# Kernel optimization log

Hardware: AMD Instinct MI355X
Metric: run time of the kernel (lower is better)

Reference implementation:

```python
import jax, jax.numpy as jnp
import numpy as np

KH, KW = 3, 3
KK = KH * KW
PAD = 1
STRIDE = 1


def setup_inputs() -> dict:
    key = jax.random.key(0)
    k1, k2, k3 = jax.random.split(key, 3)
    x = jax.random.normal(k1, (4, 64, 224, 224), jnp.float32)
    weight = jax.random.normal(k2, (64, 64, KH, KW), jnp.float32) * 0.05
    bias = jax.random.normal(k3, (64,), jnp.float32)
    return {"x": x, "weight": weight, "bias": bias}


def reference(x, weight, bias):
    B, C, H, W = x.shape
    # --- conv output (the wrapper delegates this to the wrapped conv) ---
    y = jax.lax.conv_general_dilated(
        x, weight,
        window_strides=(STRIDE, STRIDE),
        padding=((PAD, PAD), (PAD, PAD)),
        dimension_numbers=("NCHW", "OIHW", "NCHW"),
    ) + bias[None, :, None, None]

    # --- zero-count histogram (groups=1; torch code's [:, :, :, 0, 0] indexing
    # selects group 0 / out-channel 0, so only weight[0] matters) ---
    # patches: (B, C*KK, Ho, Wo), channel-major ordering (channel, then kh, kw)
    patches = jax.lax.conv_general_dilated_patches(
        x, (KH, KW), (STRIDE, STRIDE), ((PAD, PAD), (PAD, PAD)))
    Ho, Wo = patches.shape[2], patches.shape[3]
    patches = patches.reshape(B, C, KK, Ho, Wo)
    prod = patches * weight[0].reshape(1, C, KK, 1, 1)  # patch * weight, oc=0
    # num_of_zeros = kk - count_nonzero over the kernel window
    zeros = KK - jnp.count_nonzero(prod, axis=2)  # (B, C, Ho, Wo), int
    # accumulate one_hot(zeros).sum over (batch, h, w) per input channel
    zf = zeros.transpose(1, 0, 2, 3).reshape(C, -1)  # (C, B*Ho*Wo)
    hist = jnp.zeros((C, KK + 1), jnp.float32).at[
        jnp.arange(C)[:, None], zf].add(1.0)
    return y, hist
```

## Files before the change

kernel.cpp:

```cpp
#include <hip/hip_runtime.h>

#define HW 224
#define HW2 50176
#define NCH 64
#define NPIX (4 * HW2)
#define CONV_OUT_ELEMS (4 * NCH * HW2)
#define ZCAP 8192

#define TH 7
#define TW 32
#define LHH 9
#define LWW 34
#define NPOS 306
#define NGRAN (NPOS * 8)

typedef short bf16x8 __attribute__((ext_vector_type(8)));
typedef float f32x4 __attribute__((ext_vector_type(4)));

__device__ __forceinline__ unsigned short f2bf(float f) {
    unsigned u = __float_as_uint(f);
    u += 0x7FFFu + ((u >> 16) & 1u);
    return (unsigned short)(u >> 16);
}

__device__ __forceinline__ void gload16(const unsigned short* src,
                                        unsigned short* dst_uniform) {
    __builtin_amdgcn_global_load_lds(
        (const __attribute__((address_space(1))) unsigned int*)src,
        (__attribute__((address_space(3))) unsigned int*)dst_uniform,
        16, 0, 0);
}


__global__ __launch_bounds__(256) void prep_fused(
    const float* __restrict__ xf, const float* __restrict__ w,
    unsigned short* __restrict__ xbf, unsigned short* __restrict__ wbufA,
    int* __restrict__ zcnt, unsigned int* __restrict__ zlist)
{
    const int tid = threadIdx.x;
    const int bid = blockIdx.x;

    if (bid >= 6272) {
        const int o = (bid - 6272) * 256 + tid;
        if (o < 18 * 2048) {
            const int j    = o & 7;
            const int lane = (o >> 3) & 63;
            const int n    = lane & 15;
            const int q    = lane >> 4;
            const int mg   = (o >> 9) & 3;
            const int k    = o >> 11;
            const int tap  = k >> 1;
            const int half = k & 1;
            const int ci   = half * 32 + q * 8 + j;
            const int co   = mg * 16 + n;
            wbufA[o] = f2bf(w[(co * 64 + ci) * 9 + tap]);
        }
        return;
    }

    const int pix = bid * 32 + (tid >> 3);
    const int oct = tid & 7;
    const int b   = pix / HW2;
    const int rem = pix - b * HW2;
    const float* src = xf + (size_t)(b * NCH + oct * 8) * HW2 + rem;

    float fv[8];
#pragma unroll
    for (int j = 0; j < 8; ++j) fv[j] = src[(size_t)j * HW2];

    bf16x8 v;
#pragma unroll
    for (int j = 0; j < 8; ++j) v[j] = (short)f2bf(fv[j]);
    *reinterpret_cast<bf16x8*>(xbf + (size_t)pix * 64 + oct * 8) = v;

    bool anyz = false;
#pragma unroll
    for (int j = 0; j < 8; ++j) anyz |= (fv[j] == 0.0f);
    if (__builtin_expect(anyz, 0)) {
        const int yy = rem / HW;
        const int xx = rem - yy * HW;
#pragma unroll
        for (int j = 0; j < 8; ++j) {
            if (fv[j] == 0.0f) {
                const int idx = atomicAdd(zcnt, 1);
                if (idx < ZCAP) {
                    const int ci = oct * 8 + j;
                    zlist[idx] = ((unsigned)b << 22) | ((unsigned)ci << 16)
                               | ((unsigned)yy << 8) | (unsigned)xx;
                }
            }
        }
    }
}

__global__ __launch_bounds__(256, 4) void conv_fused(
    const unsigned short* __restrict__ xbf,
    const unsigned short* __restrict__ wbufA,
    const float* __restrict__ bias, float* __restrict__ y)
{
    __shared__ alignas(16) unsigned short xs[NPOS * 64];

    const int tid  = threadIdx.x;
    const int wv   = tid >> 6;
    const int lane = tid & 63;
    const int n    = lane & 15;
    const int q    = lane >> 4;
    const int c0   = blockIdx.x * TW;
    const int r0   = blockIdx.y * TH;
    const int b    = blockIdx.z;

#pragma unroll
    for (int it = 0; it < 10; ++it) {
        const int s = it * 256 + tid;
        if (it < 9 || s < NGRAN) {
            const int pos = s >> 3;
            const int bq  = s & 7;
            const int rr  = pos / LWW;
            const int cc  = pos - rr * LWW;
            const int gy  = r0 + rr - 1;
            const int gx  = c0 + cc - 1;
            const int blk = bq ^ (pos & 7);
            unsigned short* dstb = xs + (size_t)(it * 256 + wv * 64) * 8;
            if ((unsigned)gy < (unsigned)HW && (unsigned)gx < (unsigned)HW) {
                const unsigned short* src =
                    xbf + ((size_t)(b * HW + gy) * HW + gx) * 64 + blk * 8;
                gload16(src, dstb);
            } else {
                *reinterpret_cast<bf16x8*>(xs + (size_t)s * 8) =
                    (bf16x8){0, 0, 0, 0, 0, 0, 0, 0};
            }
        }
    }
    __syncthreads();

    f32x4 acc[4][4];
#pragma unroll
    for (int mg = 0; mg < 4; ++mg)
#pragma unroll
        for (int g = 0; g < 4; ++g) acc[mg][g] = (f32x4){0.f, 0.f, 0.f, 0.f};

    const int rw0 = 2 * wv;
    const int rw1 = (2 * wv + 1 > TH - 1) ? TH - 1 : 2 * wv + 1;

#pragma unroll
    for (int tap = 0; tap < 9; ++tap) {
        const int dh = tap / 3, dw = tap % 3;
#pragma unroll
        for (int half = 0; half < 2; ++half) {
            const int k = tap * 2 + half;
            bf16x8 a[4];
#pragma unroll
            for (int mg = 0; mg < 4; ++mg)
                a[mg] = *reinterpret_cast<const bf16x8*>(
                    wbufA + (k * 4 + mg) * 512 + lane * 8);
#pragma unroll
            for (int g = 0; g < 4; ++g) {
                const int rI  = (g >> 1) ? rw1 : rw0;
                const int pos = (rI + dh) * LWW + (g & 1) * 16 + dw + n;
                const int phys = pos * 8 + ((half * 4 + q) ^ (pos & 7));
                const bf16x8 bf =
                    *reinterpret_cast<const bf16x8*>(xs + phys * 8);
#pragma unroll
                for (int mg = 0; mg < 4; ++mg)
                    acc[mg][g] = __builtin_amdgcn_mfma_f32_16x16x32_bf16(
                        a[mg], bf, acc[mg][g], 0, 0, 0);
            }
        }
    }

#pragma unroll
    for (int g = 0; g < 4; ++g) {
        const int rt = 2 * wv + (g >> 1);
        if (rt < TH) {
            const int row = r0 + rt;
            const int col = c0 + (g & 1) * 16 + n;
#pragma unroll
            for (int mg = 0; mg < 4; ++mg) {
#pragma unroll
                for (int rg = 0; rg < 4; ++rg) {
                    const int co = mg * 16 + q * 4 + rg;
                    y[((size_t)(b * NCH + co) * HW + row) * HW + col] =
                        acc[mg][g][rg] + bias[co];
                }
            }
        }
    }
}

__global__ __launch_bounds__(256) void hist_final(
    const float* __restrict__ x, const float* __restrict__ w,
    const int* __restrict__ zcnt, const unsigned int* __restrict__ zlist,
    float* __restrict__ hist)
{
    __shared__ int lh[640];
    const int tid = threadIdx.x;
    for (int i = tid; i < 640; i += 256) lh[i] = 0;
    __syncthreads();

    if (tid < 64) {
        const int c = tid;
        float wk[9];
#pragma unroll
        for (int k = 0; k < 9; ++k) wk[k] = w[c * 9 + k];
        int bins[10];
#pragma unroll
        for (int k = 0; k < 10; ++k) bins[k] = 0;
#pragma unroll
        for (int rcat = 0; rcat < 3; ++rcat) {
#pragma unroll
            for (int scat = 0; scat < 3; ++scat) {
                int z = 0;
#pragma unroll
                for (int k = 0; k < 9; ++k) {
                    const int kh = k / 3, kw = k % 3;
                    const bool oob =
                        (rcat == 0 && kh == 0) || (rcat == 2 && kh == 2) ||
                        (scat == 0 && kw == 0) || (scat == 2 && kw == 2);
                    z += (oob || wk[k] == 0.0f) ? 1 : 0;
                }
                const int cnt =
                    4 * (rcat == 1 ? 222 : 1) * (scat == 1 ? 222 : 1);
                bins[z] += cnt;
            }
        }
#pragma unroll
        for (int k = 0; k < 10; ++k) lh[c * 10 + k] = bins[k];
    }
    __syncthreads();

    const int L = min(*zcnt, ZCAP);
    for (int p = tid; p < L * 9; p += 256) {
        const int e = p / 9, t = p - e * 9;
        const unsigned ent = zlist[e];
        const int b  = (int)(ent >> 22);
        const int c  = (int)(ent >> 16) & 63;
        const int zy = (int)(ent >> 8) & 255;
        const int zx = (int)ent & 255;
        const int kh = t / 3, kw = t % 3;
        const int r = zy - kh + 1, s = zx - kw + 1;
        if ((unsigned)r >= (unsigned)HW || (unsigned)s >= (unsigned)HW)
            continue;
        bool first = true;
        for (int e2 = 0; e2 < e && first; ++e2) {
            const unsigned ent2 = zlist[e2];
            if ((ent2 >> 16) == (ent >> 16)) {
                const int y2 = (int)(ent2 >> 8) & 255;
                const int x2 = (int)ent2 & 255;
                if ((unsigned)(y2 - r + 1) < 3u && (unsigned)(x2 - s + 1) < 3u)
                    first = false;
            }
        }
        if (!first) continue;

        const float* plane = x + (size_t)(b * NCH + c) * HW2;
        int zb = 0, zt = 0;
#pragma unroll
        for (int k = 0; k < 9; ++k) {
            const int kh2 = k / 3, kw2 = k % 3;
            const int yy = r + kh2 - 1, xx = s + kw2 - 1;
            const bool oob = (unsigned)yy >= (unsigned)HW ||
                             (unsigned)xx >= (unsigned)HW;
            const bool w0 = (w[c * 9 + k] == 0.0f);
            const bool x0 = !oob && (plane[yy * HW + xx] == 0.0f);
            zb += (oob || w0) ? 1 : 0;
            zt += (oob || w0 || x0) ? 1 : 0;
        }
        if (zb != zt) {
            atomicAdd(&lh[c * 10 + zb], -1);
            atomicAdd(&lh[c * 10 + zt], 1);
        }
    }
    __syncthreads();
    for (int i = tid; i < 640; i += 256) hist[i] = (float)lh[i];
}

__global__ void prep_weights_fb(const float* __restrict__ w,
                                unsigned short* __restrict__ wbuf) {
    const int o = blockIdx.x * 256 + threadIdx.x;
    if (o >= 2 * 9 * 4 * 16 * 32) return;
    const int ci = o & 31;
    const int t1 = o >> 5;
    const int co = t1 & 15;
    const int t2 = t1 >> 4;
    const int mg = t2 & 3;
    const int t3 = t2 >> 2;
    const int tap = t3 % 9;
    const int chunk = t3 / 9;
    wbuf[o] = f2bf(w[((mg * 16 + co) * 64 + (chunk * 32 + ci)) * 9 + tap]);
}

__global__ __launch_bounds__(256, 2) void conv_mfma_fb(
    const float* __restrict__ x, const unsigned short* __restrict__ wbuf,
    const float* __restrict__ bias, float* __restrict__ y)
{
    __shared__ alignas(16) unsigned short xs[340 * 32];
    const int tid  = threadIdx.x;
    const int wv   = tid >> 6;
    const int lane = tid & 63;
    const int n    = lane & 15;
    const int q    = lane >> 4;
    const int c0   = blockIdx.x * 32;
    const int r0   = blockIdx.y * 8;
    const int b    = blockIdx.z;

    f32x4 acc[4][4];
#pragma unroll
    for (int mg = 0; mg < 4; ++mg)
#pragma unroll
        for (int g = 0; g < 4; ++g) acc[mg][g] = (f32x4){0.f, 0.f, 0.f, 0.f};

    for (int chunk = 0; chunk < 2; ++chunk) {
        if (chunk) __syncthreads();
        const int ci0 = chunk * 32;
        for (int i = tid; i < 1360; i += 256) {
            const int ci8 = i / 340;
            const int pos = i - ci8 * 340;
            const int r   = pos / 34;
            const int c   = pos - r * 34;
            const int gy  = r0 + r - 1;
            const int gx  = c0 + c - 1;
            bf16x8 v;
            if ((unsigned)gy < (unsigned)HW && (unsigned)gx < (unsigned)HW) {
                const float* src =
                    x + ((size_t)(b * NCH + ci0 + ci8 * 8) * HW + gy) * HW + gx;
#pragma unroll
                for (int j = 0; j < 8; ++j) v[j] = (short)f2bf(src[(size_t)j * HW2]);
            } else {
#pragma unroll
                for (int j = 0; j < 8; ++j) v[j] = 0;
            }
            *reinterpret_cast<bf16x8*>(&xs[pos * 32 + ci8 * 8]) = v;
        }
        __syncthreads();

#pragma unroll
        for (int tap = 0; tap < 9; ++tap) {
            const int dh = tap / 3, dw = tap % 3;
            bf16x8 a[4];
#pragma unroll
            for (int mg = 0; mg < 4; ++mg) {
                const unsigned short* ap =
                    wbuf + ((chunk * 9 + tap) * 4 + mg) * 512 + n * 32 + q * 8;
                a[mg] = *reinterpret_cast<const bf16x8*>(ap);
            }
#pragma unroll
            for (int g = 0; g < 4; ++g) {
                const int rl = 2 * wv + (g >> 1) + dh;
                const int cl = (g & 1) * 16 + dw + n;
                const bf16x8 bf =
                    *reinterpret_cast<const bf16x8*>(&xs[(rl * 34 + cl) * 32 + q * 8]);
#pragma unroll
                for (int mg = 0; mg < 4; ++mg)
                    acc[mg][g] = __builtin_amdgcn_mfma_f32_16x16x32_bf16(
                        a[mg], bf, acc[mg][g], 0, 0, 0);
            }
        }
    }

#pragma unroll
    for (int g = 0; g < 4; ++g) {
        const int row = r0 + 2 * wv + (g >> 1);
        const int col = c0 + (g & 1) * 16 + n;
#pragma unroll
        for (int mg = 0; mg < 4; ++mg) {
#pragma unroll
            for (int rg = 0; rg < 4; ++rg) {
                const int co = mg * 16 + q * 4 + rg;
                y[((size_t)(b * NCH + co) * HW + row) * HW + col] =
                    acc[mg][g][rg] + bias[co];
            }
        }
    }
}

__global__ __launch_bounds__(256) void hist_v2(
    const float* __restrict__ x, const float* __restrict__ w,
    float* __restrict__ hist)
{
    __shared__ int lh[10];
    const int tid = threadIdx.x;
    const int col = tid;
    const int rg  = blockIdx.x;
    const int c   = blockIdx.y;
    const int b   = blockIdx.z;
    if (tid < 10) lh[tid] = 0;
    __syncthreads();

    int h[10];
#pragma unroll
    for (int k = 0; k < 10; ++k) h[k] = 0;

    if (col < HW) {
        const float* plane = x + (size_t)(b * NCH + c) * HW2;
        float wk[9];
#pragma unroll
        for (int k = 0; k < 9; ++k) wk[k] = w[c * 9 + k];

        const bool vl = col > 0, vr = col < HW - 1;
        const int r0 = rg * 28;
        float u0, u1, u2, m0, m1, m2;
        if (r0 > 0) {
            const float* p = plane + (size_t)(r0 - 1) * HW + col;
            u0 = vl ? p[-1] : 0.f; u1 = p[0]; u2 = vr ? p[1] : 0.f;
        } else { u0 = u1 = u2 = 0.f; }
        {
            const float* p = plane + (size_t)r0 * HW + col;
            m0 = vl ? p[-1] : 0.f; m1 = p[0]; m2 = vr ? p[1] : 0.f;
        }

        for (int r = r0; r < r0 + 28; ++r) {
            float d0, d1, d2;
            if (r + 1 < HW) {
                const float* p = plane + (size_t)(r + 1) * HW + col;
                d0 = vl ? p[-1] : 0.f; d1 = p[0]; d2 = vr ? p[1] : 0.f;
            } else { d0 = d1 = d2 = 0.f; }

            int cnt = 0;
            cnt += (u0 * wk[0] != 0.f); cnt += (u1 * wk[1] != 0.f); cnt += (u2 * wk[2] != 0.f);
            cnt += (m0 * wk[3] != 0.f); cnt += (m1 * wk[4] != 0.f); cnt += (m2 * wk[5] != 0.f);
            cnt += (d0 * wk[6] != 0.f); cnt += (d1 * wk[7] != 0.f); cnt += (d2 * wk[8] != 0.f);
            const int z = 9 - cnt;
#pragma unroll
            for (int k = 0; k < 10; ++k) h[k] += (z == k);
            u0 = m0; u1 = m1; u2 = m2; m0 = d0; m1 = d1; m2 = d2;
        }
    }

#pragma unroll
    for (int k = 0; k < 10; ++k) {
        int v = h[k];
        v += __shfl_xor(v, 32); v += __shfl_xor(v, 16); v += __shfl_xor(v, 8);
        v += __shfl_xor(v, 4);  v += __shfl_xor(v, 2);  v += __shfl_xor(v, 1);
        if ((tid & 63) == 0 && v != 0) atomicAdd(&lh[k], v);
    }
    __syncthreads();
    if (tid < 10 && lh[tid] > 0)
        atomicAdd(&hist[c * 10 + tid], (float)lh[tid]);
}

extern "C" void kernel_launch(void* const* d_in, const int* in_sizes, int n_in,
                              void* d_out, int out_size, void* d_ws, size_t ws_size,
                              hipStream_t stream) {
    const float* x    = (const float*)d_in[0];
    const float* w    = (const float*)d_in[1];
    const float* bias = (const float*)d_in[2];
    float* y    = (float*)d_out;
    float* hist = (float*)d_out + CONV_OUT_ELEMS;

    const size_t XBF_OFF = 73728;
    const size_t ZC_OFF  = XBF_OFF + (size_t)NPIX * 64 * 2;
    const size_t ZL_OFF  = ZC_OFF + 64;
    const size_t NEED    = ZL_OFF + (size_t)ZCAP * 4;

    if (ws_size >= NEED) {
        unsigned short* wbufA = (unsigned short*)d_ws;
        unsigned short* xbf   = (unsigned short*)((char*)d_ws + XBF_OFF);
        int* zcnt             = (int*)((char*)d_ws + ZC_OFF);
        unsigned int* zlist   = (unsigned int*)((char*)d_ws + ZL_OFF);

        hipMemsetAsync(zcnt, 0, sizeof(int), stream);
        prep_fused<<<6416, 256, 0, stream>>>(x, w, xbf, wbufA, zcnt, zlist);
        conv_fused<<<dim3(7, 32, 4), 256, 0, stream>>>(xbf, wbufA, bias, y);
        hist_final<<<1, 256, 0, stream>>>(x, w, zcnt, zlist, hist);
    } else {
        hipMemsetAsync(hist, 0, 64 * 10 * sizeof(float), stream);
        unsigned short* wbuf = (unsigned short*)d_ws;
        prep_weights_fb<<<144, 256, 0, stream>>>(w, wbuf);
        conv_mfma_fb<<<dim3(7, 28, 4), 256, 0, stream>>>(x, wbuf, bias, y);
        hist_v2<<<dim3(8, 64, 4), 256, 0, stream>>>(x, w, hist);
    }
}
```

Before: 132.9 us.

## Halve conv tile width, swizzle block order, vectorize prep loads over pixel pairs

The conv kernel tile shrinks from 32 to 16 columns, which halves the accumulators per wave and the LDS footprint so occupancy can rise from 4 to 7 blocks per CU. The grid becomes 1D with an XCD-aware remapping of block index to tile. The prep kernel now handles two adjacent pixels per thread using float2 loads, halving its block count. The trade-off is more halo reloading per output and fewer MFMAs per LDS load.

```diff
diff --git a/kernel.cpp b/kernel.cpp
--- a/kernel.cpp
+++ b/kernel.cpp
@@ -8,10 +8,10 @@
 #define ZCAP 8192
 
 #define TH 7
-#define TW 32
+#define TW 16
 #define LHH 9
-#define LWW 34
-#define NPOS 306
+#define LWW 18
+#define NPOS 162
 #define NGRAN (NPOS * 8)
 
 typedef short bf16x8 __attribute__((ext_vector_type(8)));
@@ -40,8 +40,8 @@
     const int tid = threadIdx.x;
     const int bid = blockIdx.x;
 
-    if (bid >= 6272) {
-        const int o = (bid - 6272) * 256 + tid;
+    if (bid >= 3136) {
+        const int o = (bid - 3136) * 256 + tid;
         if (o < 18 * 2048) {
             const int j    = o & 7;
             const int lane = (o >> 3) & 63;
@@ -58,42 +58,52 @@
         return;
     }
 
-    const int pix = bid * 32 + (tid >> 3);
-    const int oct = tid & 7;
-    const int b   = pix / HW2;
-    const int rem = pix - b * HW2;
+    const int pair = bid * 32 + (tid >> 3);
+    const int oct  = tid & 7;
+    const int pix  = pair * 2;
+    const int b    = pix / HW2;
+    const int rem  = pix - b * HW2;
     const float* src = xf + (size_t)(b * NCH + oct * 8) * HW2 + rem;
 
-    float fv[8];
-#pragma unroll
-    for (int j = 0; j < 8; ++j) fv[j] = src[(size_t)j * HW2];
-
-    bf16x8 v;
-#pragma unroll
-    for (int j = 0; j < 8; ++j) v[j] = (short)f2bf(fv[j]);
-    *reinterpret_cast<bf16x8*>(xbf + (size_t)pix * 64 + oct * 8) = v;
-
+    float2 fv[8];
+#pragma unroll
+    for (int j = 0; j < 8; ++j)
+        fv[j] = *reinterpret_cast<const float2*>(src + (size_t)j * HW2);
+
+    bf16x8 v0, v1;
     bool anyz = false;
 #pragma unroll
-    for (int j = 0; j < 8; ++j) anyz |= (fv[j] == 0.0f);
+    for (int j = 0; j < 8; ++j) {
+        v0[j] = (short)f2bf(fv[j].x);
+        v1[j] = (short)f2bf(fv[j].y);
+        anyz |= (fv[j].x == 0.0f) | (fv[j].y == 0.0f);
+    }
+    *reinterpret_cast<bf16x8*>(xbf + (size_t)pix * 64 + oct * 8) = v0;
+    *reinterpret_cast<bf16x8*>(xbf + (size_t)(pix + 1) * 64 + oct * 8) = v1;
+
     if (__builtin_expect(anyz, 0)) {
-        const int yy = rem / HW;
-        const int xx = rem - yy * HW;
-#pragma unroll
-        for (int j = 0; j < 8; ++j) {
-            if (fv[j] == 0.0f) {
-                const int idx = atomicAdd(zcnt, 1);
-                if (idx < ZCAP) {
-                    const int ci = oct * 8 + j;
-                    zlist[idx] = ((unsigned)b << 22) | ((unsigned)ci << 16)
-                               | ((unsigned)yy << 8) | (unsigned)xx;
+#pragma unroll
+        for (int pp = 0; pp < 2; ++pp) {
+            const int rr = rem + pp;
+            const int yy = rr / HW;
+            const int xx = rr - yy * HW;
+#pragma unroll
+            for (int j = 0; j < 8; ++j) {
+                const float f = pp ? fv[j].y : fv[j].x;
+                if (f == 0.0f) {
+                    const int idx = atomicAdd(zcnt, 1);
+                    if (idx < ZCAP) {
+                        const int ci = oct * 8 + j;
+                        zlist[idx] = ((unsigned)b << 22) | ((unsigned)ci << 16)
+                                   | ((unsigned)yy << 8) | (unsigned)xx;
+                    }
                 }
             }
         }
     }
 }
 
-__global__ __launch_bounds__(256, 4) void conv_fused(
+__global__ __launch_bounds__(256, 7) void conv_fused(
     const unsigned short* __restrict__ xbf,
     const unsigned short* __restrict__ wbufA,
     const float* __restrict__ bias, float* __restrict__ y)
@@ -105,14 +115,20 @@
     const int lane = tid & 63;
     const int n    = lane & 15;
     const int q    = lane >> 4;
-    const int c0   = blockIdx.x * TW;
-    const int r0   = blockIdx.y * TH;
-    const int b    = blockIdx.z;
-
-#pragma unroll
-    for (int it = 0; it < 10; ++it) {
+
+    const int phys_b = blockIdx.x;
+    const int l   = (phys_b & 7) * 224 + (phys_b >> 3);
+    const int b   = l / 448;
+    const int rm  = l - b * 448;
+    const int ct  = rm >> 5;
+    const int rt  = rm & 31;
+    const int c0  = ct * TW;
+    const int r0  = rt * TH;
+
+#pragma unroll
+    for (int it = 0; it < 6; ++it) {
         const int s = it * 256 + tid;
-        if (it < 9 || s < NGRAN) {
+        if (it < 5 || s < NGRAN) {
             const int pos = s >> 3;
             const int bq  = s & 7;
             const int rr  = pos / LWW;
@@ -133,11 +149,11 @@
     }
     __syncthreads();
 
-    f32x4 acc[4][4];
+    f32x4 acc[4][2];
 #pragma unroll
     for (int mg = 0; mg < 4; ++mg)
 #pragma unroll
-        for (int g = 0; g < 4; ++g) acc[mg][g] = (f32x4){0.f, 0.f, 0.f, 0.f};
+        for (int g = 0; g < 2; ++g) acc[mg][g] = (f32x4){0.f, 0.f, 0.f, 0.f};
 
     const int rw0 = 2 * wv;
     const int rw1 = (2 * wv + 1 > TH - 1) ? TH - 1 : 2 * wv + 1;
@@ -154,9 +170,9 @@
                 a[mg] = *reinterpret_cast<const bf16x8*>(
                     wbufA + (k * 4 + mg) * 512 + lane * 8);
 #pragma unroll
-            for (int g = 0; g < 4; ++g) {
-                const int rI  = (g >> 1) ? rw1 : rw0;
-                const int pos = (rI + dh) * LWW + (g & 1) * 16 + dw + n;
+            for (int g = 0; g < 2; ++g) {
+                const int rI  = g ? rw1 : rw0;
+                const int pos = (rI + dh) * LWW + dw + n;
                 const int phys = pos * 8 + ((half * 4 + q) ^ (pos & 7));
                 const bf16x8 bf =
                     *reinterpret_cast<const bf16x8*>(xs + phys * 8);
@@ -169,11 +185,11 @@
     }
 
 #pragma unroll
-    for (int g = 0; g < 4; ++g) {
-        const int rt = 2 * wv + (g >> 1);
-        if (rt < TH) {
-            const int row = r0 + rt;
-            const int col = c0 + (g & 1) * 16 + n;
+    for (int g = 0; g < 2; ++g) {
+        const int rtile = 2 * wv + g;
+        if (rtile < TH) {
+            const int row = r0 + rtile;
+            const int col = c0 + n;
 #pragma unroll
             for (int mg = 0; mg < 4; ++mg) {
 #pragma unroll
@@ -459,8 +475,8 @@
         unsigned int* zlist   = (unsigned int*)((char*)d_ws + ZL_OFF);
 
         hipMemsetAsync(zcnt, 0, sizeof(int), stream);
-        prep_fused<<<6416, 256, 0, stream>>>(x, w, xbf, wbufA, zcnt, zlist);
-        conv_fused<<<dim3(7, 32, 4), 256, 0, stream>>>(xbf, wbufA, bias, y);
+        prep_fused<<<3280, 256, 0, stream>>>(x, w, xbf, wbufA, zcnt, zlist);
+        conv_fused<<<1792, 256, 0, stream>>>(xbf, wbufA, bias, y);
         hist_final<<<1, 256, 0, stream>>>(x, w, zcnt, zlist, hist);
     } else {
         hipMemsetAsync(hist, 0, 64 * 10 * sizeof(float), stream);
```

Result: slower. 161.2 us (+21.3%).

## Vectorize prep loads to float4 per thread and remap conv blocks XCD-aware

Applied to the files above, without the earlier changes.

The prep kernel now has each thread load float4 (four consecutive pixels) per channel instead of scalar floats, converts them to bf16 and writes four 16-byte vectors. The block count drops by four, and the zero detection walks all four pixels. The conv kernel switches to a 1D grid and remaps block IDs so that consecutive logical tiles land on the same XCD (phys&7 chunking), which is meant to improve L2 reuse of halo rows. The remap assumes round-robin dispatch across 8 XCDs.

```diff
diff --git a/kernel.cpp b/kernel.cpp
--- a/kernel.cpp
+++ b/kernel.cpp
@@ -40,8 +40,8 @@
     const int tid = threadIdx.x;
     const int bid = blockIdx.x;
 
-    if (bid >= 6272) {
-        const int o = (bid - 6272) * 256 + tid;
+    if (bid >= 1568) {
+        const int o = (bid - 1568) * 256 + tid;
         if (o < 18 * 2048) {
             const int j    = o & 7;
             const int lane = (o >> 3) & 63;
@@ -58,35 +58,51 @@
         return;
     }
 
-    const int pix = bid * 32 + (tid >> 3);
-    const int oct = tid & 7;
-    const int b   = pix / HW2;
-    const int rem = pix - b * HW2;
+    const int quad = bid * 32 + (tid >> 3);
+    const int oct  = tid & 7;
+    const int pix  = quad * 4;
+    const int b    = pix / HW2;
+    const int rem  = pix - b * HW2;
     const float* src = xf + (size_t)(b * NCH + oct * 8) * HW2 + rem;
 
-    float fv[8];
-#pragma unroll
-    for (int j = 0; j < 8; ++j) fv[j] = src[(size_t)j * HW2];
-
-    bf16x8 v;
-#pragma unroll
-    for (int j = 0; j < 8; ++j) v[j] = (short)f2bf(fv[j]);
-    *reinterpret_cast<bf16x8*>(xbf + (size_t)pix * 64 + oct * 8) = v;
-
+    float4 fv[8];
+#pragma unroll
+    for (int j = 0; j < 8; ++j)
+        fv[j] = *reinterpret_cast<const float4*>(src + (size_t)j * HW2);
+
+    bf16x8 v[4];
     bool anyz = false;
 #pragma unroll
-    for (int j = 0; j < 8; ++j) anyz |= (fv[j] == 0.0f);
+    for (int j = 0; j < 8; ++j) {
+        v[0][j] = (short)f2bf(fv[j].x);
+        v[1][j] = (short)f2bf(fv[j].y);
+        v[2][j] = (short)f2bf(fv[j].z);
+        v[3][j] = (short)f2bf(fv[j].w);
+        anyz |= (fv[j].x == 0.0f) | (fv[j].y == 0.0f) |
+                (fv[j].z == 0.0f) | (fv[j].w == 0.0f);
+    }
+#pragma unroll
+    for (int pp = 0; pp < 4; ++pp)
+        *reinterpret_cast<bf16x8*>(xbf + (size_t)(pix + pp) * 64 + oct * 8) =
+            v[pp];
+
     if (__builtin_expect(anyz, 0)) {
-        const int yy = rem / HW;
-        const int xx = rem - yy * HW;
-#pragma unroll
-        for (int j = 0; j < 8; ++j) {
-            if (fv[j] == 0.0f) {
-                const int idx = atomicAdd(zcnt, 1);
-                if (idx < ZCAP) {
-                    const int ci = oct * 8 + j;
-                    zlist[idx] = ((unsigned)b << 22) | ((unsigned)ci << 16)
-                               | ((unsigned)yy << 8) | (unsigned)xx;
+#pragma unroll
+        for (int pp = 0; pp < 4; ++pp) {
+            const int rr = rem + pp;
+            const int yy = rr / HW;
+            const int xx = rr - yy * HW;
+#pragma unroll
+            for (int j = 0; j < 8; ++j) {
+                const float f = pp == 0 ? fv[j].x : pp == 1 ? fv[j].y
+                              : pp == 2 ? fv[j].z : fv[j].w;
+                if (f == 0.0f) {
+                    const int idx = atomicAdd(zcnt, 1);
+                    if (idx < ZCAP) {
+                        const int ci = oct * 8 + j;
+                        zlist[idx] = ((unsigned)b << 22) | ((unsigned)ci << 16)
+                                   | ((unsigned)yy << 8) | (unsigned)xx;
+                    }
                 }
             }
         }
@@ -105,9 +121,15 @@
     const int lane = tid & 63;
     const int n    = lane & 15;
     const int q    = lane >> 4;
-    const int c0   = blockIdx.x * TW;
-    const int r0   = blockIdx.y * TH;
-    const int b    = blockIdx.z;
+
+    const int phys_b = blockIdx.x;
+    const int l   = (phys_b & 7) * 112 + (phys_b >> 3);
+    const int b   = l / 224;
+    const int rm  = l - b * 224;
+    const int ct  = rm >> 5;
+    const int rt  = rm & 31;
+    const int c0  = ct * TW;
+    const int r0  = rt * TH;
 
 #pragma unroll
     for (int it = 0; it < 10; ++it) {
@@ -170,9 +192,9 @@
 
 #pragma unroll
     for (int g = 0; g < 4; ++g) {
-        const int rt = 2 * wv + (g >> 1);
-        if (rt < TH) {
-            const int row = r0 + rt;
+        const int rtile = 2 * wv + (g >> 1);
+        if (rtile < TH) {
+            const int row = r0 + rtile;
             const int col = c0 + (g & 1) * 16 + n;
 #pragma unroll
             for (int mg = 0; mg < 4; ++mg) {
@@ -459,8 +481,8 @@
         unsigned int* zlist   = (unsigned int*)((char*)d_ws + ZL_OFF);
 
         hipMemsetAsync(zcnt, 0, sizeof(int), stream);
-        prep_fused<<<6416, 256, 0, stream>>>(x, w, xbf, wbufA, zcnt, zlist);
-        conv_fused<<<dim3(7, 32, 4), 256, 0, stream>>>(xbf, wbufA, bias, y);
+        prep_fused<<<1712, 256, 0, stream>>>(x, w, xbf, wbufA, zcnt, zlist);
+        conv_fused<<<896, 256, 0, stream>>>(xbf, wbufA, bias, y);
         hist_final<<<1, 256, 0, stream>>>(x, w, zcnt, zlist, hist);
     } else {
         hipMemsetAsync(hist, 0, 64 * 10 * sizeof(float), stream);
```

Result: faster. 125.6 us (-5.5%).
